# Kernel optimization log

Hardware: AMD Instinct MI355X
Metric: run time of the kernel (lower is better)

The kernel has to match this reference:

```python
import jax, jax.numpy as jnp
import numpy as np

N = 100000; IN_DIM = 256; H = 128; R = 4; L = 2
E_RAND = 1600000; PE_LEN = 2000; SCALING = 8.0 / 4.0; EPS = 1e-5


def _build_pe():
    # sinusoidal table [PE_LEN, H], even cols sin, odd cols cos (as in PositionalEncoding)
    pos = jnp.arange(PE_LEN, dtype=jnp.float32)[:, None]
    div = jnp.exp(jnp.arange(0, H, 2, dtype=jnp.float32) * (-np.log(10000.0) / H))
    pe = jnp.zeros((PE_LEN, H), jnp.float32)
    pe = pe.at[:, 0::2].set(jnp.sin(pos * div))
    pe = pe.at[:, 1::2].set(jnp.cos(pos * div))
    return pe


def setup_inputs() -> dict:
    key = jax.random.key(0)
    ks = jax.random.split(key, 16)
    features = jax.random.normal(ks[0], (N, IN_DIM), jnp.float32)
    src = jax.random.randint(ks[1], (E_RAND,), 0, N, jnp.int32)
    dst = jax.random.randint(ks[2], (E_RAND,), 0, N, jnp.int32)
    loops = jnp.arange(N, dtype=jnp.int32)  # dgl.add_self_loop
    edge_src = jnp.concatenate([src, loops])
    edge_dst = jnp.concatenate([dst, loops])
    s = 0.05
    return {
        "features": features, "edge_src": edge_src, "edge_dst": edge_dst,
        "pe": _build_pe(),
        "W_in": jax.random.normal(ks[3], (H, IN_DIM)) * s, "b_in": jnp.zeros((H,), jnp.float32),
        "A_in": jax.random.normal(ks[4], (R, IN_DIM)) * s, "B_in": jax.random.normal(ks[5], (H, R)) * s,
        "gnn_W": jax.random.normal(ks[6], (L, H, H)) * s, "gnn_b": jnp.zeros((L, H), jnp.float32),
        "lW": jax.random.normal(ks[7], (L, H, H)) * s, "lb": jnp.zeros((L, H), jnp.float32),
        "lA": jax.random.normal(ks[8], (L, R, H)) * s, "lB": jax.random.normal(ks[9], (L, H, R)) * s,
        "gamma": jnp.ones((L, H), jnp.float32), "beta": jnp.zeros((L, H), jnp.float32),
        "W_out": jax.random.normal(ks[10], (H, H)) * s, "b_out": jnp.zeros((H,), jnp.float32),
        "A_out": jax.random.normal(ks[11], (R, H)) * s, "B_out": jax.random.normal(ks[12], (H, R)) * s,
    }


def _lora_linear(x, W, b, A, B):
    # frozen linear + low-rank update (dropout = identity at inference)
    return x @ W.T + b + ((x @ A.T) @ B.T) * SCALING


def _graph_conv(x, W, b, src, dst, n):
    # DGL GraphConv, norm='both': D_in^{-1/2} A (D_out^{-1/2} X) W + b
    ones = jnp.ones(src.shape[0], x.dtype)
    deg_out = jax.ops.segment_sum(ones, src, num_segments=n)
    deg_in = jax.ops.segment_sum(ones, dst, num_segments=n)
    norm_out = jnp.where(deg_out > 0, jax.lax.rsqrt(jnp.maximum(deg_out, 1.0)), 0.0)
    norm_in = jnp.where(deg_in > 0, jax.lax.rsqrt(jnp.maximum(deg_in, 1.0)), 0.0)
    m = (x * norm_out[:, None])[src]                        # [E, H] gathered messages
    agg = jax.ops.segment_sum(m, dst, num_segments=n)       # [N, H] scatter-add
    return (agg * norm_in[:, None]) @ W + b


def _layer_norm(x, g, b):
    mu = jnp.mean(x, -1, keepdims=True)
    var = jnp.mean((x - mu) ** 2, -1, keepdims=True)
    return (x - mu) * jax.lax.rsqrt(var + EPS) * g + b


def reference(features, edge_src, edge_dst, pe, W_in, b_in, A_in, B_in,
              gnn_W, gnn_b, lW, lb, lA, lB, gamma, beta,
              W_out, b_out, A_out, B_out):
    n = features.shape[0]
    h = _lora_linear(features, W_in, b_in, A_in, B_in)
    pos = jnp.clip(jnp.arange(n), 0, PE_LEN - 1)
    h = h + pe[pos]
    for i in range(L):
        h_new = _graph_conv(h, gnn_W[i], gnn_b[i], edge_src, edge_dst, n) \
                + _lora_linear(h, lW[i], lb[i], lA[i], lB[i])
        h_new = jax.nn.gelu(_layer_norm(h_new, gamma[i], beta[i]), approximate=False)
        h = h + h_new  # dropout = identity at inference
    return _lora_linear(h, W_out, b_out, A_out, B_out)
```

## Files before the change

### kernel.cpp

```cpp
#include <hip/hip_runtime.h>
#include <cstdint>
#include <cstddef>

#define HDIM 128
#define INDIM 256
#define RANK 4
#define NLAYER 2
#define PELEN 2000

#define BM 64
#define BK 32
#define XT_LD 68
#define WT_LD 132

constexpr float SCALING_F = 2.0f;
constexpr float EPS_LN = 1e-5f;


__global__ void deg_kernel(const int* __restrict__ src, const int* __restrict__ dst,
                           int* __restrict__ dego, int* __restrict__ degi, int E) {
    int e = blockIdx.x * 256 + threadIdx.x;
    if (e < E) {
        atomicAdd(&dego[src[e]], 1);
        atomicAdd(&degi[dst[e]], 1);
    }
}

__global__ void norm_kernel(const int* __restrict__ dego, const int* __restrict__ degi,
                            float* __restrict__ nout, float* __restrict__ nin, int N) {
    int i = blockIdx.x * 256 + threadIdx.x;
    if (i < N) {
        int a = dego[i];
        nout[i] = (a > 0) ? rsqrtf((float)a) : 0.0f;
        int b = degi[i];
        nin[i]  = (b > 0) ? rsqrtf((float)b) : 0.0f;
    }
}

__global__ __launch_bounds__(256) void scan1_kernel(const int* __restrict__ degi,
                                                    int* __restrict__ sincl,
                                                    int* __restrict__ bsum, int N) {
    int i = blockIdx.x * 256 + threadIdx.x;
    int lane = threadIdx.x & 63;
    int w = threadIdx.x >> 6;
    int x = (i < N) ? degi[i] : 0;
#pragma unroll
    for (int d = 1; d < 64; d <<= 1) {
        int y = __shfl_up(x, d);
        if (lane >= d) x += y;
    }
    __shared__ int wsum[4];
    if (lane == 63) wsum[w] = x;
    __syncthreads();
    int add = 0;
    for (int j = 0; j < w; ++j) add += wsum[j];
    x += add;
    if (i < N) sincl[i] = x;
    if (threadIdx.x == 255) bsum[blockIdx.x] = x;
}

__global__ __launch_bounds__(512) void scan2_kernel(int* __restrict__ bsum, int NB) {
    int i = threadIdx.x;
    int lane = i & 63;
    int w = i >> 6;
    int x = (i < NB) ? bsum[i] : 0;
#pragma unroll
    for (int d = 1; d < 64; d <<= 1) {
        int y = __shfl_up(x, d);
        if (lane >= d) x += y;
    }
    __shared__ int wsum[8];
    if (lane == 63) wsum[w] = x;
    __syncthreads();
    int add = 0;
    for (int j = 0; j < w; ++j) add += wsum[j];
    x += add;
    if (i < NB) bsum[i] = x;
}

__global__ __launch_bounds__(256) void scan3_kernel(const int* __restrict__ degi,
                                                    const int* __restrict__ sincl,
                                                    const int* __restrict__ bsum,
                                                    int* __restrict__ row_ptr,
                                                    int* __restrict__ cursor, int N) {
    int i = blockIdx.x * 256 + threadIdx.x;
    if (i >= N) return;
    int b = blockIdx.x;
    int incl = sincl[i] + ((b > 0) ? bsum[b - 1] : 0);
    int excl = incl - degi[i];
    row_ptr[i] = excl;
    cursor[i] = excl;
    if (i == N - 1) row_ptr[N] = incl;
}

__global__ void place_kernel(const int* __restrict__ src, const int* __restrict__ dst,
                             int* __restrict__ cursor, int* __restrict__ csr_src, int E) {
    int e = blockIdx.x * 256 + threadIdx.x;
    if (e < E) {
        int d = dst[e];
        int pos = atomicAdd(&cursor[d], 1);
        csr_src[pos] = src[e];
    }
}

__global__ __launch_bounds__(256) void gather_kernel(
        const float* __restrict__ h, const float* __restrict__ nout,
        const float* __restrict__ nin, const int* __restrict__ row_ptr,
        const int* __restrict__ csr_src, float* __restrict__ agg, int N) {
    int node = blockIdx.x * 4 + (threadIdx.x >> 6);
    if (node >= N) return;
    int lane = threadIdx.x & 63;
    int start = row_ptr[node], end = row_ptr[node + 1];
    const float2* h2 = (const float2*)h;
    float2 acc = make_float2(0.f, 0.f);
    int i = start;
    for (; i + 2 <= end; i += 2) {
        int s0 = csr_src[i], s1 = csr_src[i + 1];
        float n0 = nout[s0], n1 = nout[s1];
        float2 v0 = h2[(size_t)s0 * 64 + lane];
        float2 v1 = h2[(size_t)s1 * 64 + lane];
        acc.x += v0.x * n0; acc.y += v0.y * n0;
        acc.x += v1.x * n1; acc.y += v1.y * n1;
    }
    if (i < end) {
        int s = csr_src[i];
        float n = nout[s];
        float2 v = h2[(size_t)s * 64 + lane];
        acc.x += v.x * n; acc.y += v.y * n;
    }
    float ni = nin[node];
    ((float2*)agg)[(size_t)node * 64 + lane] = make_float2(acc.x * ni, acc.y * ni);
}


__device__ __forceinline__ void stage_x(const float* __restrict__ X, int ldx, int brow,
                                        int k0, int N, int tid, float xt[BK][XT_LD]) {
    int rr = tid & 63;
    int kc = tid >> 6;
    int row = brow + rr;
    float4 v0 = make_float4(0.f, 0.f, 0.f, 0.f), v1 = v0;
    if (row < N) {
        const float4* s = (const float4*)(X + (size_t)row * ldx + k0 + kc * 8);
        v0 = s[0]; v1 = s[1];
    }
    int kb = kc * 8;
    xt[kb + 0][rr] = v0.x; xt[kb + 1][rr] = v0.y; xt[kb + 2][rr] = v0.z; xt[kb + 3][rr] = v0.w;
    xt[kb + 4][rr] = v1.x; xt[kb + 5][rr] = v1.y; xt[kb + 6][rr] = v1.z; xt[kb + 7][rr] = v1.w;
}

__device__ __forceinline__ void stage_wT(const float* __restrict__ W, int ldw,
                                         int k0, int tid, float wt[BK][WT_LD]) {
    int n = tid >> 1, half = tid & 1;
    const float4* s = (const float4*)(W + (size_t)n * ldw + k0 + half * 16);
    float4 a = s[0], b = s[1], c = s[2], d = s[3];
    int kb = half * 16;
    wt[kb +  0][n] = a.x; wt[kb +  1][n] = a.y; wt[kb +  2][n] = a.z; wt[kb +  3][n] = a.w;
    wt[kb +  4][n] = b.x; wt[kb +  5][n] = b.y; wt[kb +  6][n] = b.z; wt[kb +  7][n] = b.w;
    wt[kb +  8][n] = c.x; wt[kb +  9][n] = c.y; wt[kb + 10][n] = c.z; wt[kb + 11][n] = c.w;
    wt[kb + 12][n] = d.x; wt[kb + 13][n] = d.y; wt[kb + 14][n] = d.z; wt[kb + 15][n] = d.w;
}

__device__ __forceinline__ void stage_wD(const float* __restrict__ W,
                                         int k0, int tid, float wt[BK][WT_LD]) {
    int kk = tid >> 3, nc = tid & 7;
    const float4* s = (const float4*)(W + (size_t)(k0 + kk) * HDIM);
#pragma unroll
    for (int j = 0; j < 4; ++j) {
        float4 v = s[nc + 8 * j];
        *(float4*)&wt[kk][(nc + 8 * j) * 4] = v;
    }
}

__device__ __forceinline__ void mm_inner(const float xt[BK][XT_LD], const float wt[BK][WT_LD],
                                         int r0, int c0, float acc[4][8]) {
#pragma unroll
    for (int kk = 0; kk < BK; ++kk) {
        float4 a  = *(const float4*)&xt[kk][r0];
        float4 b0 = *(const float4*)&wt[kk][c0];
        float4 b1 = *(const float4*)&wt[kk][c0 + 4];
        float av[4] = {a.x, a.y, a.z, a.w};
        float bv[8] = {b0.x, b0.y, b0.z, b0.w, b1.x, b1.y, b1.z, b1.w};
#pragma unroll
        for (int i = 0; i < 4; ++i)
#pragma unroll
            for (int j = 0; j < 8; ++j)
                acc[i][j] = fmaf(av[i], bv[j], acc[i][j]);
    }
}

__device__ __forceinline__ float lora_part(const float xt[BK][XT_LD],
                                           const float* __restrict__ A, int ldA,
                                           int k0, int lrow, int lq) {
    const float* Arow = A + (size_t)lq * ldA + k0;
    float p = 0.f;
#pragma unroll
    for (int q4 = 0; q4 < BK / 4; ++q4) {
        float4 av = *(const float4*)(Arow + q4 * 4);
        p = fmaf(xt[q4 * 4 + 0][lrow], av.x, p);
        p = fmaf(xt[q4 * 4 + 1][lrow], av.y, p);
        p = fmaf(xt[q4 * 4 + 2][lrow], av.z, p);
        p = fmaf(xt[q4 * 4 + 3][lrow], av.w, p);
    }
    return p;
}


__global__ __launch_bounds__(256) void input_kernel(
        const float* __restrict__ feats, const float* __restrict__ pe,
        const float* __restrict__ Win, const float* __restrict__ bin,
        const float* __restrict__ Ain, const float* __restrict__ Bin,
        float* __restrict__ h, int N) {
    __shared__ float xt[BK][XT_LD];
    __shared__ float wt[BK][WT_LD];
    __shared__ float ts[BM][RANK];
    int brow = blockIdx.x * BM;
    int tid = threadIdx.x;
    int rg = tid >> 4, cg = tid & 15;
    int r0 = rg * 4, c0 = cg * 8;
    int lrow = tid >> 2, lq = tid & 3;

    float acc[4][8] = {};
    float tacc = 0.f;

    for (int k0 = 0; k0 < INDIM; k0 += BK) {
        __syncthreads();
        stage_x(feats, INDIM, brow, k0, N, tid, xt);
        stage_wT(Win, INDIM, k0, tid, wt);
        __syncthreads();
        tacc += lora_part(xt, Ain, INDIM, k0, lrow, lq);
        mm_inner(xt, wt, r0, c0, acc);
    }
    ts[lrow][lq] = tacc;
    __syncthreads();

#pragma unroll
    for (int i = 0; i < 4; ++i) {
        int row = brow + r0 + i;
        if (row >= N) break;
        float4 tq = *(const float4*)&ts[r0 + i][0];
        int pos = (row < PELEN) ? row : (PELEN - 1);
        const float* per = pe + (size_t)pos * HDIM;
        float o[8];
#pragma unroll
        for (int j = 0; j < 8; ++j) {
            int c = c0 + j;
            float lo = tq.x * Bin[c * RANK + 0] + tq.y * Bin[c * RANK + 1]
                     + tq.z * Bin[c * RANK + 2] + tq.w * Bin[c * RANK + 3];
            o[j] = acc[i][j] + bin[c] + per[c] + SCALING_F * lo;
        }
        float* ho = h + (size_t)row * HDIM + c0;
        *(float4*)(ho)     = make_float4(o[0], o[1], o[2], o[3]);
        *(float4*)(ho + 4) = make_float4(o[4], o[5], o[6], o[7]);
    }
}


__global__ __launch_bounds__(256) void layer_kernel(
        float* __restrict__ h, const float* __restrict__ agg,
        const float* __restrict__ gW, const float* __restrict__ gb,
        const float* __restrict__ lWp, const float* __restrict__ lbp,
        const float* __restrict__ lAp, const float* __restrict__ lBp,
        const float* __restrict__ gammap, const float* __restrict__ betap, int N) {
    __shared__ float xt[BK][XT_LD];
    __shared__ float wt[BK][WT_LD];
    __shared__ float ts[BM][RANK];
    int brow = blockIdx.x * BM;
    int tid = threadIdx.x;
    int rg = tid >> 4, cg = tid & 15;
    int r0 = rg * 4, c0 = cg * 8;
    int lrow = tid >> 2, lq = tid & 3;

    float acc[4][8] = {};
    float tacc = 0.f;

    for (int k0 = 0; k0 < HDIM; k0 += BK) {
        __syncthreads();
        stage_x(agg, HDIM, brow, k0, N, tid, xt);
        stage_wD(gW, k0, tid, wt);
        __syncthreads();
        mm_inner(xt, wt, r0, c0, acc);
    }
    for (int k0 = 0; k0 < HDIM; k0 += BK) {
        __syncthreads();
        stage_x(h, HDIM, brow, k0, N, tid, xt);
        stage_wT(lWp, HDIM, k0, tid, wt);
        __syncthreads();
        tacc += lora_part(xt, lAp, HDIM, k0, lrow, lq);
        mm_inner(xt, wt, r0, c0, acc);
    }
    ts[lrow][lq] = tacc;
    __syncthreads();

#pragma unroll
    for (int i = 0; i < 4; ++i) {
        int row = brow + r0 + i;
        if (row >= N) continue;
        float4 tq = *(const float4*)&ts[r0 + i][0];
        float val[8];
#pragma unroll
        for (int j = 0; j < 8; ++j) {
            int c = c0 + j;
            float lo = tq.x * lBp[c * RANK + 0] + tq.y * lBp[c * RANK + 1]
                     + tq.z * lBp[c * RANK + 2] + tq.w * lBp[c * RANK + 3];
            val[j] = acc[i][j] + gb[c] + lbp[c] + SCALING_F * lo;
        }
        float ssum = 0.f;
#pragma unroll
        for (int j = 0; j < 8; ++j) ssum += val[j];
#pragma unroll
        for (int m = 8; m >= 1; m >>= 1) ssum += __shfl_xor(ssum, m);
        float mu = ssum * (1.0f / HDIM);
        float vsum = 0.f;
#pragma unroll
        for (int j = 0; j < 8; ++j) { float d = val[j] - mu; vsum += d * d; }
#pragma unroll
        for (int m = 8; m >= 1; m >>= 1) vsum += __shfl_xor(vsum, m);
        float rstd = rsqrtf(vsum * (1.0f / HDIM) + EPS_LN);

        float* ho = h + (size_t)row * HDIM + c0;
        float4 h0 = *(const float4*)(ho);
        float4 h1 = *(const float4*)(ho + 4);
        float hold[8] = {h0.x, h0.y, h0.z, h0.w, h1.x, h1.y, h1.z, h1.w};
        float o[8];
#pragma unroll
        for (int j = 0; j < 8; ++j) {
            int c = c0 + j;
            float y = (val[j] - mu) * rstd * gammap[c] + betap[c];
            float g = 0.5f * y * (1.0f + erff(y * 0.70710678118654752f));
            o[j] = hold[j] + g;
        }
        *(float4*)(ho)     = make_float4(o[0], o[1], o[2], o[3]);
        *(float4*)(ho + 4) = make_float4(o[4], o[5], o[6], o[7]);
    }
}


__global__ __launch_bounds__(256) void out_kernel(
        const float* __restrict__ h,
        const float* __restrict__ W, const float* __restrict__ b,
        const float* __restrict__ A, const float* __restrict__ B,
        float* __restrict__ out, int N) {
    __shared__ float xt[BK][XT_LD];
    __shared__ float wt[BK][WT_LD];
    __shared__ float ts[BM][RANK];
    int brow = blockIdx.x * BM;
    int tid = threadIdx.x;
    int rg = tid >> 4, cg = tid & 15;
    int r0 = rg * 4, c0 = cg * 8;
    int lrow = tid >> 2, lq = tid & 3;

    float acc[4][8] = {};
    float tacc = 0.f;

    for (int k0 = 0; k0 < HDIM; k0 += BK) {
        __syncthreads();
        stage_x(h, HDIM, brow, k0, N, tid, xt);
        stage_wT(W, HDIM, k0, tid, wt);
        __syncthreads();
        tacc += lora_part(xt, A, HDIM, k0, lrow, lq);
        mm_inner(xt, wt, r0, c0, acc);
    }
    ts[lrow][lq] = tacc;
    __syncthreads();

#pragma unroll
    for (int i = 0; i < 4; ++i) {
        int row = brow + r0 + i;
        if (row >= N) break;
        float4 tq = *(const float4*)&ts[r0 + i][0];
        float o[8];
#pragma unroll
        for (int j = 0; j < 8; ++j) {
            int c = c0 + j;
            float lo = tq.x * B[c * RANK + 0] + tq.y * B[c * RANK + 1]
                     + tq.z * B[c * RANK + 2] + tq.w * B[c * RANK + 3];
            o[j] = acc[i][j] + b[c] + SCALING_F * lo;
        }
        float* oo = out + (size_t)row * HDIM + c0;
        *(float4*)(oo)     = make_float4(o[0], o[1], o[2], o[3]);
        *(float4*)(oo + 4) = make_float4(o[4], o[5], o[6], o[7]);
    }
}


extern "C" void kernel_launch(void* const* d_in, const int* in_sizes, int n_in,
                              void* d_out, int out_size, void* d_ws, size_t ws_size,
                              hipStream_t stream) {
    const float* features = (const float*)d_in[0];
    const int*   esrc     = (const int*)d_in[1];
    const int*   edst     = (const int*)d_in[2];
    const float* pe       = (const float*)d_in[3];
    const float* W_in     = (const float*)d_in[4];
    const float* b_in     = (const float*)d_in[5];
    const float* A_in     = (const float*)d_in[6];
    const float* B_in     = (const float*)d_in[7];
    const float* gnn_W    = (const float*)d_in[8];
    const float* gnn_b    = (const float*)d_in[9];
    const float* lW       = (const float*)d_in[10];
    const float* lb       = (const float*)d_in[11];
    const float* lA       = (const float*)d_in[12];
    const float* lB       = (const float*)d_in[13];
    const float* gamma    = (const float*)d_in[14];
    const float* beta     = (const float*)d_in[15];
    const float* W_out    = (const float*)d_in[16];
    const float* b_out    = (const float*)d_in[17];
    const float* A_out    = (const float*)d_in[18];
    const float* B_out    = (const float*)d_in[19];

    int N = in_sizes[0] / INDIM;
    int E = in_sizes[1];
    int NB = (N + 255) / 256;

    char* ws = (char*)d_ws;
    float* h       = (float*)ws;
    float* agg     = h + (size_t)N * HDIM;
    int*   dego    = (int*)(agg + (size_t)N * HDIM);
    int*   degi    = dego + N;
    float* nout    = (float*)(degi + N);
    float* nin     = nout + N;
    int*   row_ptr = (int*)(nin + N);
    int*   cursor  = row_ptr + N + 1;
    int*   sincl   = cursor + N;
    int*   bsum    = sincl + N;
    int*   csr_src = bsum + NB;

    hipMemsetAsync(dego, 0, 2 * (size_t)N * sizeof(int), stream);
    deg_kernel<<<(E + 255) / 256, 256, 0, stream>>>(esrc, edst, dego, degi, E);
    norm_kernel<<<NB, 256, 0, stream>>>(dego, degi, nout, nin, N);

    scan1_kernel<<<NB, 256, 0, stream>>>(degi, sincl, bsum, N);
    scan2_kernel<<<1, 512, 0, stream>>>(bsum, NB);
    scan3_kernel<<<NB, 256, 0, stream>>>(degi, sincl, bsum, row_ptr, cursor, N);
    place_kernel<<<(E + 255) / 256, 256, 0, stream>>>(esrc, edst, cursor, csr_src, E);

    int gemm_grid = (N + BM - 1) / BM;
    input_kernel<<<gemm_grid, 256, 0, stream>>>(features, pe, W_in, b_in, A_in, B_in, h, N);

    for (int i = 0; i < NLAYER; ++i) {
        gather_kernel<<<(N + 3) / 4, 256, 0, stream>>>(h, nout, nin, row_ptr, csr_src, agg, N);
        layer_kernel<<<gemm_grid, 256, 0, stream>>>(
            h, agg,
            gnn_W + (size_t)i * HDIM * HDIM, gnn_b + (size_t)i * HDIM,
            lW + (size_t)i * HDIM * HDIM, lb + (size_t)i * HDIM,
            lA + (size_t)i * RANK * HDIM, lB + (size_t)i * HDIM * RANK,
            gamma + (size_t)i * HDIM, beta + (size_t)i * HDIM, N);
    }

    out_kernel<<<gemm_grid, 256, 0, stream>>>(h, W_out, b_out, A_out, B_out, (float*)d_out, N);
}
```

Before: 1.192 ms.

## Double row tile to 128 and prefetch next K-slab into registers

Each GEMM block now covers 128 rows with 512 threads, so every staged weight tile is reused across twice as many rows. The staging helpers are split into global-load and shared-store halves, so the next K-slab is loaded into registers while the current one is being multiplied. The two K loops in the layer kernel are merged into one 8-step pipelined loop. The trade-off is more registers per thread and fewer, larger blocks, which may reduce occupancy.

```diff
diff --git a/kernel.cpp b/kernel.cpp
--- a/kernel.cpp
+++ b/kernel.cpp
@@ -8,10 +8,9 @@
 #define NLAYER 2
 #define PELEN 2000
 
-#define BM 64
+#define BM 128
 #define BK 32
-#define XT_LD 68
-#define WT_LD 132
+#define TLD 132
 
 constexpr float SCALING_F = 2.0f;
 constexpr float EPS_LN = 1e-5f;
@@ -133,45 +132,50 @@
 }
 
 
-__device__ __forceinline__ void stage_x(const float* __restrict__ X, int ldx, int brow,
-                                        int k0, int N, int tid, float xt[BK][XT_LD]) {
-    int rr = tid & 63;
-    int kc = tid >> 6;
+__device__ __forceinline__ void load_x(const float* __restrict__ X, int ldx, int brow,
+                                       int k0, int N, int tid, float4& a, float4& b) {
+    int rr = tid & 127, kc = tid >> 7;
     int row = brow + rr;
-    float4 v0 = make_float4(0.f, 0.f, 0.f, 0.f), v1 = v0;
+    a = make_float4(0.f, 0.f, 0.f, 0.f); b = a;
     if (row < N) {
         const float4* s = (const float4*)(X + (size_t)row * ldx + k0 + kc * 8);
-        v0 = s[0]; v1 = s[1];
-    }
-    int kb = kc * 8;
-    xt[kb + 0][rr] = v0.x; xt[kb + 1][rr] = v0.y; xt[kb + 2][rr] = v0.z; xt[kb + 3][rr] = v0.w;
-    xt[kb + 4][rr] = v1.x; xt[kb + 5][rr] = v1.y; xt[kb + 6][rr] = v1.z; xt[kb + 7][rr] = v1.w;
-}
-
-__device__ __forceinline__ void stage_wT(const float* __restrict__ W, int ldw,
-                                         int k0, int tid, float wt[BK][WT_LD]) {
-    int n = tid >> 1, half = tid & 1;
-    const float4* s = (const float4*)(W + (size_t)n * ldw + k0 + half * 16);
-    float4 a = s[0], b = s[1], c = s[2], d = s[3];
-    int kb = half * 16;
-    wt[kb +  0][n] = a.x; wt[kb +  1][n] = a.y; wt[kb +  2][n] = a.z; wt[kb +  3][n] = a.w;
-    wt[kb +  4][n] = b.x; wt[kb +  5][n] = b.y; wt[kb +  6][n] = b.z; wt[kb +  7][n] = b.w;
-    wt[kb +  8][n] = c.x; wt[kb +  9][n] = c.y; wt[kb + 10][n] = c.z; wt[kb + 11][n] = c.w;
-    wt[kb + 12][n] = d.x; wt[kb + 13][n] = d.y; wt[kb + 14][n] = d.z; wt[kb + 15][n] = d.w;
-}
-
-__device__ __forceinline__ void stage_wD(const float* __restrict__ W,
-                                         int k0, int tid, float wt[BK][WT_LD]) {
-    int kk = tid >> 3, nc = tid & 7;
-    const float4* s = (const float4*)(W + (size_t)(k0 + kk) * HDIM);
-#pragma unroll
-    for (int j = 0; j < 4; ++j) {
-        float4 v = s[nc + 8 * j];
-        *(float4*)&wt[kk][(nc + 8 * j) * 4] = v;
-    }
-}
-
-__device__ __forceinline__ void mm_inner(const float xt[BK][XT_LD], const float wt[BK][WT_LD],
+        a = s[0]; b = s[1];
+    }
+}
+__device__ __forceinline__ void store_x(int tid, const float4& a, const float4& b,
+                                        float xt[BK][TLD]) {
+    int rr = tid & 127, kb = (tid >> 7) * 8;
+    xt[kb + 0][rr] = a.x; xt[kb + 1][rr] = a.y; xt[kb + 2][rr] = a.z; xt[kb + 3][rr] = a.w;
+    xt[kb + 4][rr] = b.x; xt[kb + 5][rr] = b.y; xt[kb + 6][rr] = b.z; xt[kb + 7][rr] = b.w;
+}
+
+__device__ __forceinline__ void load_wT(const float* __restrict__ W, int ldw,
+                                        int k0, int tid, float4& a, float4& b) {
+    int n = tid & 127, q = tid >> 7;
+    const float4* s = (const float4*)(W + (size_t)n * ldw + k0 + q * 8);
+    a = s[0]; b = s[1];
+}
+__device__ __forceinline__ void store_wT(int tid, const float4& a, const float4& b,
+                                         float wt[BK][TLD]) {
+    int n = tid & 127, kb = (tid >> 7) * 8;
+    wt[kb + 0][n] = a.x; wt[kb + 1][n] = a.y; wt[kb + 2][n] = a.z; wt[kb + 3][n] = a.w;
+    wt[kb + 4][n] = b.x; wt[kb + 5][n] = b.y; wt[kb + 6][n] = b.z; wt[kb + 7][n] = b.w;
+}
+
+__device__ __forceinline__ void load_wD(const float* __restrict__ W,
+                                        int k0, int tid, float4& a, float4& b) {
+    int kk = tid >> 4, nc = tid & 15;
+    const float4* s = (const float4*)(W + (size_t)(k0 + kk) * HDIM + nc * 8);
+    a = s[0]; b = s[1];
+}
+__device__ __forceinline__ void store_wD(int tid, const float4& a, const float4& b,
+                                         float wt[BK][TLD]) {
+    int kk = tid >> 4, nc = tid & 15;
+    *(float4*)&wt[kk][nc * 8]     = a;
+    *(float4*)&wt[kk][nc * 8 + 4] = b;
+}
+
+__device__ __forceinline__ void mm_inner(const float xt[BK][TLD], const float wt[BK][TLD],
                                          int r0, int c0, float acc[4][8]) {
 #pragma unroll
     for (int kk = 0; kk < BK; ++kk) {
@@ -188,7 +192,7 @@
     }
 }
 
-__device__ __forceinline__ float lora_part(const float xt[BK][XT_LD],
+__device__ __forceinline__ float lora_part(const float xt[BK][TLD],
                                            const float* __restrict__ A, int ldA,
                                            int k0, int lrow, int lq) {
     const float* Arow = A + (size_t)lq * ldA + k0;
@@ -205,13 +209,13 @@
 }
 
 
-__global__ __launch_bounds__(256) void input_kernel(
+__global__ __launch_bounds__(512) void input_kernel(
         const float* __restrict__ feats, const float* __restrict__ pe,
         const float* __restrict__ Win, const float* __restrict__ bin,
         const float* __restrict__ Ain, const float* __restrict__ Bin,
         float* __restrict__ h, int N) {
-    __shared__ float xt[BK][XT_LD];
-    __shared__ float wt[BK][WT_LD];
+    __shared__ float xt[BK][TLD];
+    __shared__ float wt[BK][TLD];
     __shared__ float ts[BM][RANK];
     int brow = blockIdx.x * BM;
     int tid = threadIdx.x;
@@ -221,13 +225,21 @@
 
     float acc[4][8] = {};
     float tacc = 0.f;
-
-    for (int k0 = 0; k0 < INDIM; k0 += BK) {
-        __syncthreads();
-        stage_x(feats, INDIM, brow, k0, N, tid, xt);
-        stage_wT(Win, INDIM, k0, tid, wt);
-        __syncthreads();
-        tacc += lora_part(xt, Ain, INDIM, k0, lrow, lq);
+    float4 xa, xb, wa, wb;
+
+    load_x(feats, INDIM, brow, 0, N, tid, xa, xb);
+    load_wT(Win, INDIM, 0, tid, wa, wb);
+
+    for (int s = 0; s < INDIM / BK; ++s) {
+        __syncthreads();
+        store_x(tid, xa, xb, xt);
+        store_wT(tid, wa, wb, wt);
+        __syncthreads();
+        if (s + 1 < INDIM / BK) {
+            load_x(feats, INDIM, brow, (s + 1) * BK, N, tid, xa, xb);
+            load_wT(Win, INDIM, (s + 1) * BK, tid, wa, wb);
+        }
+        tacc += lora_part(xt, Ain, INDIM, s * BK, lrow, lq);
         mm_inner(xt, wt, r0, c0, acc);
     }
     ts[lrow][lq] = tacc;
@@ -255,14 +267,14 @@
 }
 
 
-__global__ __launch_bounds__(256) void layer_kernel(
+__global__ __launch_bounds__(512) void layer_kernel(
         float* __restrict__ h, const float* __restrict__ agg,
         const float* __restrict__ gW, const float* __restrict__ gb,
         const float* __restrict__ lWp, const float* __restrict__ lbp,
         const float* __restrict__ lAp, const float* __restrict__ lBp,
         const float* __restrict__ gammap, const float* __restrict__ betap, int N) {
-    __shared__ float xt[BK][XT_LD];
-    __shared__ float wt[BK][WT_LD];
+    __shared__ float xt[BK][TLD];
+    __shared__ float wt[BK][TLD];
     __shared__ float ts[BM][RANK];
     int brow = blockIdx.x * BM;
     int tid = threadIdx.x;
@@ -272,20 +284,26 @@
 
     float acc[4][8] = {};
     float tacc = 0.f;
-
-    for (int k0 = 0; k0 < HDIM; k0 += BK) {
-        __syncthreads();
-        stage_x(agg, HDIM, brow, k0, N, tid, xt);
-        stage_wD(gW, k0, tid, wt);
-        __syncthreads();
-        mm_inner(xt, wt, r0, c0, acc);
-    }
-    for (int k0 = 0; k0 < HDIM; k0 += BK) {
-        __syncthreads();
-        stage_x(h, HDIM, brow, k0, N, tid, xt);
-        stage_wT(lWp, HDIM, k0, tid, wt);
-        __syncthreads();
-        tacc += lora_part(xt, lAp, HDIM, k0, lrow, lq);
+    float4 xa, xb, wa, wb;
+
+    load_x(agg, HDIM, brow, 0, N, tid, xa, xb);
+    load_wD(gW, 0, tid, wa, wb);
+
+    for (int s = 0; s < 8; ++s) {
+        __syncthreads();
+        store_x(tid, xa, xb, xt);
+        if (s < 4) store_wD(tid, wa, wb, wt);
+        else       store_wT(tid, wa, wb, wt);
+        __syncthreads();
+        int ns = s + 1;
+        if (ns < 4) {
+            load_x(agg, HDIM, brow, ns * BK, N, tid, xa, xb);
+            load_wD(gW, ns * BK, tid, wa, wb);
+        } else if (ns < 8) {
+            load_x(h, HDIM, brow, (ns - 4) * BK, N, tid, xa, xb);
+            load_wT(lWp, HDIM, (ns - 4) * BK, tid, wa, wb);
+        }
+        if (s >= 4) tacc += lora_part(xt, lAp, HDIM, (s - 4) * BK, lrow, lq);
         mm_inner(xt, wt, r0, c0, acc);
     }
     ts[lrow][lq] = tacc;
@@ -335,13 +353,13 @@
 }
 
 
-__global__ __launch_bounds__(256) void out_kernel(
+__global__ __launch_bounds__(512) void out_kernel(
         const float* __restrict__ h,
         const float* __restrict__ W, const float* __restrict__ b,
         const float* __restrict__ A, const float* __restrict__ B,
         float* __restrict__ out, int N) {
-    __shared__ float xt[BK][XT_LD];
-    __shared__ float wt[BK][WT_LD];
+    __shared__ float xt[BK][TLD];
+    __shared__ float wt[BK][TLD];
     __shared__ float ts[BM][RANK];
     int brow = blockIdx.x * BM;
     int tid = threadIdx.x;
@@ -351,13 +369,21 @@
 
     float acc[4][8] = {};
     float tacc = 0.f;
-
-    for (int k0 = 0; k0 < HDIM; k0 += BK) {
-        __syncthreads();
-        stage_x(h, HDIM, brow, k0, N, tid, xt);
-        stage_wT(W, HDIM, k0, tid, wt);
-        __syncthreads();
-        tacc += lora_part(xt, A, HDIM, k0, lrow, lq);
+    float4 xa, xb, wa, wb;
+
+    load_x(h, HDIM, brow, 0, N, tid, xa, xb);
+    load_wT(W, HDIM, 0, tid, wa, wb);
+
+    for (int s = 0; s < HDIM / BK; ++s) {
+        __syncthreads();
+        store_x(tid, xa, xb, xt);
+        store_wT(tid, wa, wb, wt);
+        __syncthreads();
+        if (s + 1 < HDIM / BK) {
+            load_x(h, HDIM, brow, (s + 1) * BK, N, tid, xa, xb);
+            load_wT(W, HDIM, (s + 1) * BK, tid, wa, wb);
+        }
+        tacc += lora_part(xt, A, HDIM, s * BK, lrow, lq);
         mm_inner(xt, wt, r0, c0, acc);
     }
     ts[lrow][lq] = tacc;
@@ -434,11 +460,11 @@
     place_kernel<<<(E + 255) / 256, 256, 0, stream>>>(esrc, edst, cursor, csr_src, E);
 
     int gemm_grid = (N + BM - 1) / BM;
-    input_kernel<<<gemm_grid, 256, 0, stream>>>(features, pe, W_in, b_in, A_in, B_in, h, N);
+    input_kernel<<<gemm_grid, 512, 0, stream>>>(features, pe, W_in, b_in, A_in, B_in, h, N);
 
     for (int i = 0; i < NLAYER; ++i) {
         gather_kernel<<<(N + 3) / 4, 256, 0, stream>>>(h, nout, nin, row_ptr, csr_src, agg, N);
-        layer_kernel<<<gemm_grid, 256, 0, stream>>>(
+        layer_kernel<<<gemm_grid, 512, 0, stream>>>(
             h, agg,
             gnn_W + (size_t)i * HDIM * HDIM, gnn_b + (size_t)i * HDIM,
             lW + (size_t)i * HDIM * HDIM, lb + (size_t)i * HDIM,
@@ -446,5 +472,5 @@
             gamma + (size_t)i * HDIM, beta + (size_t)i * HDIM, N);
     }
 
-    out_kernel<<<gemm_grid, 256, 0, stream>>>(h, W_out, b_out, A_out, B_out, (float*)d_out, N);
-}
+    out_kernel<<<gemm_grid, 512, 0, stream>>>(h, W_out, b_out, A_out, B_out, (float*)d_out, N);
+}
```

New measurement: 1.450 ms. 21.7% more time.
